# Optimization experiments

Hardware: AMD Instinct MI355X
Metric: run time of the kernel (lower is better)

The kernel has to match this reference:

```python
import jax, jax.numpy as jnp
import numpy as np

Q_DIM = 32
HID = 512
OFF = Q_DIM * (Q_DIM - 1) // 2  # 496 strictly-lower-triangular entries


def setup_inputs() -> dict:
    key = jax.random.key(0)
    ks = jax.random.split(key, 20)

    def w(k, shape, fan_in):
        return (jax.random.normal(k, shape, jnp.float32) / np.float32(np.sqrt(fan_in)))

    return {
        "q": jax.random.normal(ks[0], (1, Q_DIM), jnp.float32),
        "q_t": jax.random.normal(ks[1], (1, Q_DIM), jnp.float32),
        "q_tt": jax.random.normal(ks[2], (1, Q_DIM), jnp.float32),
        # L-network (torch Linear convention: y = x @ W.T + b)
        "W1": w(ks[3], (HID, Q_DIM), Q_DIM), "b1": jnp.zeros((HID,), jnp.float32),
        "W2": w(ks[4], (HID, HID), HID),     "b2": jnp.zeros((HID,), jnp.float32),
        "W3": w(ks[5], (HID, HID), HID),     "b3": jnp.zeros((HID,), jnp.float32),
        "Wd": w(ks[6], (Q_DIM, HID), HID),   "bd": jnp.zeros((Q_DIM,), jnp.float32),
        "Wo": w(ks[7], (OFF, HID), HID),     "bo": jnp.zeros((OFF,), jnp.float32),
        # g-network
        "Wg1": w(ks[8], (HID, Q_DIM), Q_DIM), "bg1": jnp.zeros((HID,), jnp.float32),
        "Wg2": w(ks[9], (HID, HID), HID),     "bg2": jnp.zeros((HID,), jnp.float32),
        "Wg3": w(ks[10], (Q_DIM, HID), HID),  "bg3": jnp.zeros((Q_DIM,), jnp.float32),
    }


def reference(q, q_t, q_tt, W1, b1, W2, b2, W3, b3, Wd, bd, Wo, bo,
              Wg1, bg1, Wg2, bg2, Wg3, bg3):
    n = Q_DIM
    # L-network forward (sigmoid MLP)
    h1 = jax.nn.sigmoid(q @ W1.T + b1)    # [1, 512]
    h2 = jax.nn.sigmoid(h1 @ W2.T + b2)   # [1, 512]
    h3 = jax.nn.sigmoid(h2 @ W3.T + b3)   # [1, 512]
    l_diag = jnp.exp(h3 @ Wd.T + bd)      # [1, n]
    l_off = h3 @ Wo.T + bo                # [1, OFF]

    # Assemble lower-triangular L. The torch loop fills the strictly-lower
    # triangle in row-major order: (1,0),(2,0),(2,1),(3,0),... == tril_indices(k=-1).
    rows, cols = jnp.tril_indices(n, -1)
    ar = jnp.arange(n)
    L = (jnp.zeros((n, n), q.dtype)
         .at[ar, ar].set(l_diag[0])
         .at[rows, cols].set(l_off[0]))

    # Analytic Jacobian chain. diag_embed(s) @ W == s[:,None] * W (row scaling).
    s1 = (h1 * (1.0 - h1))[0]             # sigmoid'
    s2 = (h2 * (1.0 - h2))[0]
    s3 = (h3 * (1.0 - h3))[0]
    dh1 = s1[:, None] * W1                # [512, n]
    dh2 = s2[:, None] * W2                # [512, 512]
    dh3 = s3[:, None] * W3                # [512, 512]
    dh4 = jnp.concatenate([l_diag[0][:, None] * Wd, Wo], axis=0)  # [n+OFF, 512]
    dl_dq = dh4 @ (dh3 @ (dh2 @ dh1))     # [n+OFF, n]

    # dL_dq[i, j, k] = d L[i,j] / d q_k  (same tril assembly, vectorized over k)
    dL_dq = (jnp.zeros((n, n, n), q.dtype)
             .at[ar, ar, :].set(dl_dq[:n])
             .at[rows, cols, :].set(dl_dq[n:]))

    qt_col = q_t.T                        # [n, 1]
    Dqt = jnp.einsum('ijk,k->ij', dL_dq, q_t[0])   # comp_3_1 / squeeze pattern
    Fjk = jnp.einsum('ijk,i->jk', dL_dq, q_t[0])   # comp_4_1 pattern
    LTqt = L.T @ qt_col                   # [n, 1]

    comp_1 = L @ (L.T @ q_tt.T)
    comp_2 = L @ (Dqt.T @ qt_col)
    comp_3 = Dqt @ LTqt
    comp_4 = Fjk @ LTqt
    comp_5 = (q_t @ (L @ Dqt.T)).T

    # g-network
    g1 = jax.nn.sigmoid(q @ Wg1.T + bg1)
    g2 = jax.nn.sigmoid(g1 @ Wg2.T + bg2)
    g = (g2 @ Wg3.T + bg3).reshape(n, 1)

    tau = comp_1 + comp_2 + comp_3 - 0.5 * comp_4 - 0.5 * comp_5 + g
    return tau.T                          # [1, n]
```

## Files before the change

kernel.cpp:

```cpp
#include <hip/hip_runtime.h>
#include <cmath>

#define NQ 32
#define H 512
#define NOFF 496
#define NR4 528
#define NBLK 34

__device__ __forceinline__ float sigmoidf(float x) {
    return 1.0f / (1.0f + __expf(-x));
}
__device__ __forceinline__ float dot4(float4 a, float4 b) {
    return a.x * b.x + a.y * b.y + a.z * b.z + a.w * b.w;
}
__device__ __forceinline__ float ldagent(const float* p) {
    return __hip_atomic_load(p, __ATOMIC_RELAXED, __HIP_MEMORY_SCOPE_AGENT);
}
__device__ __forceinline__ float red16(float a) {
    a += __shfl_xor(a, 1, 64);
    a += __shfl_xor(a, 2, 64);
    a += __shfl_xor(a, 4, 64);
    a += __shfl_xor(a, 8, 64);
    return a;
}

__global__ void __launch_bounds__(1024, 1) fused(
    const float* __restrict__ q, const float* __restrict__ q_t, const float* __restrict__ q_tt,
    const float* __restrict__ W1, const float* __restrict__ b1,
    const float* __restrict__ W2, const float* __restrict__ b2,
    const float* __restrict__ W3, const float* __restrict__ b3,
    const float* __restrict__ Wd, const float* __restrict__ bd,
    const float* __restrict__ Wo, const float* __restrict__ bo,
    const float* __restrict__ Wg1, const float* __restrict__ bg1,
    const float* __restrict__ Wg2, const float* __restrict__ bg2,
    const float* __restrict__ Wg3, const float* __restrict__ bg3,
    float* __restrict__ U, float* __restrict__ gvec,
    unsigned* __restrict__ done, float* __restrict__ out)
{
    const int c = blockIdx.x;
    const int tid = threadIdx.x;
    const int lane = tid & 63, w = tid >> 6;
    const int p = lane & 15, rg = lane >> 4;
    const bool isg = (c == NBLK - 1);

    __shared__ float qs[NQ];
    __shared__ float hv[H], bvv[H], hv2[H], bv2[H];
    __shared__ float ldiag[NQ], loff[NOFF], vv[NR4];
    __shared__ float Lm[NQ][NQ + 1], Dq[NQ][NQ + 1], Fj[NQ][NQ + 1];
    __shared__ float qts[NQ], qtts[NQ], LTq[NQ], t1s[NQ], u2[NQ];
    __shared__ int amLast;

    if (tid < NQ) qs[tid] = q[tid];
    __syncthreads();

    if (tid < H) {
        const float* Wf = isg ? Wg1 : W1;
        const float* bf = isg ? bg1 : b1;
        const float4* wr = (const float4*)(Wf + tid * NQ);
        float acc = 0.f;
        #pragma unroll
        for (int cc = 0; cc < 8; ++cc) {
            float4 wv4 = wr[cc];
            acc += wv4.x * qs[4*cc] + wv4.y * qs[4*cc+1] + wv4.z * qs[4*cc+2] + wv4.w * qs[4*cc+3];
        }
        float h = sigmoidf(acc + bf[tid]);
        hv[tid] = h;
        bvv[tid] = (c == 0 || isg) ? h : h * (1.f - h) * Wf[tid * NQ + (c - 1)];
    }
    __syncthreads();

    {
        const float4* hv4 = (const float4*)hv;
        const float4* bv4 = (const float4*)bvv;
        float4 bh[8], bb[8];
        #pragma unroll
        for (int i = 0; i < 8; ++i) { bh[i] = hv4[p + 16*i]; bb[i] = bv4[p + 16*i]; }
        const float4* Wv = (const float4*)(isg ? Wg2 : W2);
        const float* bias = isg ? bg2 : b2;
        #pragma unroll 2
        for (int pass = 0; pass < 8; ++pass) {
            int r = w * 32 + pass * 4 + rg;
            const float4* wr = Wv + (size_t)r * (H / 4);
            float4 wreg[8];
            #pragma unroll
            for (int i = 0; i < 8; ++i) wreg[i] = wr[p + 16*i];
            float aH = 0.f, aB = 0.f;
            #pragma unroll
            for (int i = 0; i < 8; ++i) { aH += dot4(wreg[i], bh[i]); aB += dot4(wreg[i], bb[i]); }
            aH = red16(aH);
            aB = red16(aB);
            if (p == 0) {
                float h2 = sigmoidf(aH + bias[r]);
                hv2[r] = h2;
                bv2[r] = (c == 0 || isg) ? h2 : h2 * (1.f - h2) * aB;
            }
        }
    }
    __syncthreads();

    if (!isg) {
        const float4* hv4 = (const float4*)hv2;
        const float4* bv4 = (const float4*)bv2;
        float4 bh[8], bb[8];
        #pragma unroll
        for (int i = 0; i < 8; ++i) { bh[i] = hv4[p + 16*i]; bb[i] = bv4[p + 16*i]; }
        #pragma unroll 2
        for (int pass = 0; pass < 8; ++pass) {
            int r = w * 32 + pass * 4 + rg;
            const float4* wr = (const float4*)W3 + (size_t)r * (H / 4);
            float4 wreg[8];
            #pragma unroll
            for (int i = 0; i < 8; ++i) wreg[i] = wr[p + 16*i];
            float aH = 0.f, aB = 0.f;
            #pragma unroll
            for (int i = 0; i < 8; ++i) { aH += dot4(wreg[i], bh[i]); aB += dot4(wreg[i], bb[i]); }
            aH = red16(aH);
            aB = red16(aB);
            if (p == 0) {
                float h3 = sigmoidf(aH + b3[r]);
                hv[r] = h3;
                bvv[r] = (c == 0) ? h3 : h3 * (1.f - h3) * aB;
            }
        }
    } else {
        const float4* hv4 = (const float4*)hv2;
        float4 bh[8];
        #pragma unroll
        for (int i = 0; i < 8; ++i) bh[i] = hv4[p + 16*i];
        if (w < 8) {
            int r = w * 4 + rg;
            const float4* wr = (const float4*)Wg3 + (size_t)r * (H / 4);
            float4 wreg[8];
            #pragma unroll
            for (int i = 0; i < 8; ++i) wreg[i] = wr[p + 16*i];
            float aH = 0.f;
            #pragma unroll
            for (int i = 0; i < 8; ++i) aH += dot4(wreg[i], bh[i]);
            aH = red16(aH);
            if (p == 0) gvec[r] = aH + bg3[r];
        }
    }
    __syncthreads();

    if (!isg) {
        const float4* bv4 = (const float4*)bvv;
        float4 bb[8];
        #pragma unroll
        for (int i = 0; i < 8; ++i) bb[i] = bv4[p + 16*i];
        #pragma unroll 2
        for (int pass = 0; pass < 9; ++pass) {
            int r = pass * 64 + w * 4 + rg;
            if (r < NR4) {
                const float4* wr = (r < NQ) ? ((const float4*)Wd + (size_t)r * (H / 4))
                                            : ((const float4*)Wo + (size_t)(r - NQ) * (H / 4));
                float4 wreg[8];
                #pragma unroll
                for (int i = 0; i < 8; ++i) wreg[i] = wr[p + 16*i];
                float aB = 0.f;
                #pragma unroll
                for (int i = 0; i < 8; ++i) aB += dot4(wreg[i], bb[i]);
                aB = red16(aB);
                if (p == 0) U[c * NR4 + r] = aB;
            }
        }
    }

    __threadfence();
    __syncthreads();
    if (tid == 0) {
        unsigned old = __hip_atomic_fetch_add(done, 1u, __ATOMIC_ACQ_REL, __HIP_MEMORY_SCOPE_AGENT);
        amLast = (old == NBLK - 1) ? 1 : 0;
    }
    __syncthreads();
    if (!amLast) return;

    if (tid < NQ) {
        ldiag[tid] = __expf(ldagent(&U[tid]) + bd[tid]);
        qts[tid]  = q_t[tid];
        qtts[tid] = q_tt[tid];
    }
    for (int r = tid; r < NOFF; r += 1024)
        loff[r] = ldagent(&U[NQ + r]) + bo[r];
    __syncthreads();
    for (int m = tid; m < NR4; m += 1024) {
        float acc = 0.f;
        #pragma unroll
        for (int kk = 0; kk < NQ; ++kk)
            acc += ldagent(&U[(kk + 1) * NR4 + m]) * qts[kk];
        vv[m] = (m < NQ) ? ldiag[m] * acc : acc;
    }
    for (int pp = tid; pp < NQ * NQ; pp += 1024) {
        int i = pp >> 5, j = pp & 31;
        Lm[i][j] = (i == j) ? ldiag[i]
                 : (j < i ? loff[i * (i - 1) / 2 + j] : 0.f);
    }
    for (int pp = tid; pp < NQ * NQ; pp += 1024) {
        int j = pp >> 5, kk = pp & 31;
        const float* Uc = U + (kk + 1) * NR4;
        float acc = qts[j] * ldiag[j] * ldagent(&Uc[j]);
        for (int i = j + 1; i < NQ; ++i)
            acc += qts[i] * ldagent(&Uc[NQ + i * (i - 1) / 2 + j]);
        Fj[j][kk] = acc;
    }
    __syncthreads();
    for (int pp = tid; pp < NQ * NQ; pp += 1024) {
        int i = pp >> 5, j = pp & 31;
        Dq[i][j] = (i == j) ? vv[i]
                 : (j < i ? vv[NQ + i * (i - 1) / 2 + j] : 0.f);
    }
    if (tid < NQ) {
        int kcol = tid;
        float a = 0.f, bsum = 0.f;
        #pragma unroll
        for (int j = 0; j < NQ; ++j) {
            a    += Lm[j][kcol] * qts[j];
            bsum += Lm[j][kcol] * qtts[j];
        }
        LTq[kcol] = a;
        t1s[kcol] = bsum;
    }
    __syncthreads();
    if (tid < NQ) {
        int kcol = tid;
        float a = 0.f;
        #pragma unroll
        for (int j = 0; j < NQ; ++j) a += Dq[j][kcol] * qts[j];
        u2[kcol] = a;
    }
    __syncthreads();
    if (tid < NQ) {
        int i = tid;
        float c1 = 0.f, c2 = 0.f, c3 = 0.f, c4 = 0.f;
        #pragma unroll
        for (int kk = 0; kk < NQ; ++kk) {
            c1 += Lm[i][kk] * t1s[kk];
            c2 += Lm[i][kk] * u2[kk];
            c3 += Dq[i][kk] * LTq[kk];
            c4 += Fj[i][kk] * LTq[kk];
        }
        out[i] = c1 + c2 + 0.5f * c3 - 0.5f * c4 + ldagent(&gvec[i]);
    }
}

extern "C" void kernel_launch(void* const* d_in, const int* in_sizes, int n_in,
                              void* d_out, int out_size, void* d_ws, size_t ws_size,
                              hipStream_t stream) {
    const float* q    = (const float*)d_in[0];
    const float* q_t  = (const float*)d_in[1];
    const float* q_tt = (const float*)d_in[2];
    const float* W1   = (const float*)d_in[3];
    const float* b1   = (const float*)d_in[4];
    const float* W2   = (const float*)d_in[5];
    const float* b2   = (const float*)d_in[6];
    const float* W3   = (const float*)d_in[7];
    const float* b3   = (const float*)d_in[8];
    const float* Wd   = (const float*)d_in[9];
    const float* bd   = (const float*)d_in[10];
    const float* Wo   = (const float*)d_in[11];
    const float* bo   = (const float*)d_in[12];
    const float* Wg1  = (const float*)d_in[13];
    const float* bg1  = (const float*)d_in[14];
    const float* Wg2  = (const float*)d_in[15];
    const float* bg2  = (const float*)d_in[16];
    const float* Wg3  = (const float*)d_in[17];
    const float* bg3  = (const float*)d_in[18];

    float* ws = (float*)d_ws;
    float* U       = ws;
    float* gvec    = ws + 17424;
    unsigned* done = (unsigned*)(ws + 17456);
    float* out     = (float*)d_out;

    hipMemsetAsync(done, 0, sizeof(unsigned), stream);
    hipLaunchKernelGGL(fused, dim3(NBLK), dim3(1024), 0, stream,
                       q, q_t, q_tt, W1, b1, W2, b2, W3, b3,
                       Wd, bd, Wo, bo, Wg1, bg1, Wg2, bg2, Wg3, bg3,
                       U, gvec, done, out);
}
```

Before: 151.0 us.

## Split fused kernel into three layer kernels spread across 8x more blocks

Replaces the single 34-block kernel, in which each block runs the whole three-layer chain for one Jacobian column, with three kernels (ka, kb, kc). Each kernel splits a layer's output rows into 8 row blocks per column, giving 264 to 272 blocks of 256 threads. This spreads the weight-streaming matvecs across far more compute units. Layer activations and Jacobian columns now round-trip through global workspace between launches, and the forward value and the derivative products are computed in separate passes. The cost is two extra kernel launches plus the intermediate global traffic.

```diff
diff --git a/kernel.cpp b/kernel.cpp
--- a/kernel.cpp
+++ b/kernel.cpp
@@ -5,7 +5,6 @@
 #define H 512
 #define NOFF 496
 #define NR4 528
-#define NBLK 34
 
 __device__ __forceinline__ float sigmoidf(float x) {
     return 1.0f / (1.0f + __expf(-x));
@@ -24,143 +23,179 @@
     return a;
 }
 
-__global__ void __launch_bounds__(1024, 1) fused(
-    const float* __restrict__ q, const float* __restrict__ q_t, const float* __restrict__ q_tt,
+__global__ void __launch_bounds__(256) ka(
+    const float* __restrict__ q,
     const float* __restrict__ W1, const float* __restrict__ b1,
     const float* __restrict__ W2, const float* __restrict__ b2,
-    const float* __restrict__ W3, const float* __restrict__ b3,
-    const float* __restrict__ Wd, const float* __restrict__ bd,
-    const float* __restrict__ Wo, const float* __restrict__ bo,
     const float* __restrict__ Wg1, const float* __restrict__ bg1,
     const float* __restrict__ Wg2, const float* __restrict__ bg2,
-    const float* __restrict__ Wg3, const float* __restrict__ bg3,
-    float* __restrict__ U, float* __restrict__ gvec,
-    unsigned* __restrict__ done, float* __restrict__ out)
+    float* __restrict__ Y, float* __restrict__ g2)
 {
-    const int c = blockIdx.x;
+    const int c = blockIdx.x >> 3, rb = blockIdx.x & 7;
     const int tid = threadIdx.x;
     const int lane = tid & 63, w = tid >> 6;
     const int p = lane & 15, rg = lane >> 4;
-    const bool isg = (c == NBLK - 1);
+    const bool isg = (c == 33);
 
     __shared__ float qs[NQ];
-    __shared__ float hv[H], bvv[H], hv2[H], bv2[H];
+    __shared__ float bcol[H];
+
+    if (tid < NQ) qs[tid] = q[tid];
+    __syncthreads();
+
+    const float* Wf = isg ? Wg1 : W1;
+    const float* bf = isg ? bg1 : b1;
+    for (int j = tid; j < H; j += 256) {
+        const float4* wr = (const float4*)(Wf + j * NQ);
+        float acc = 0.f;
+        #pragma unroll
+        for (int cc = 0; cc < 8; ++cc) {
+            float4 wv = wr[cc];
+            acc += wv.x * qs[4*cc] + wv.y * qs[4*cc+1] + wv.z * qs[4*cc+2] + wv.w * qs[4*cc+3];
+        }
+        float h = sigmoidf(acc + bf[j]);
+        bcol[j] = (c == 0 || isg) ? h : h * (1.f - h) * Wf[j * NQ + (c - 1)];
+    }
+    __syncthreads();
+
+    const float4* b4 = (const float4*)bcol;
+    float4 bb[8];
+    #pragma unroll
+    for (int i = 0; i < 8; ++i) bb[i] = b4[p + 16 * i];
+
+    const float4* Wv = (const float4*)(isg ? Wg2 : W2);
+    const int r0 = rb * 64;
+    #pragma unroll 2
+    for (int pass = 0; pass < 4; ++pass) {
+        int r = r0 + pass * 16 + w * 4 + rg;
+        const float4* wr = Wv + (size_t)r * (H / 4);
+        float4 wreg[8];
+        #pragma unroll
+        for (int i = 0; i < 8; ++i) wreg[i] = wr[p + 16 * i];
+        float a = 0.f;
+        #pragma unroll
+        for (int i = 0; i < 8; ++i) a += dot4(wreg[i], bb[i]);
+        a = red16(a);
+        if (p == 0) {
+            if (c == 0)      Y[r] = sigmoidf(a + b2[r]);
+            else if (!isg)   Y[c * H + r] = a;
+            else             g2[r] = sigmoidf(a + bg2[r]);
+        }
+    }
+}
+
+__global__ void __launch_bounds__(256) kb(
+    const float* __restrict__ W3, const float* __restrict__ b3,
+    const float* __restrict__ Wg3, const float* __restrict__ bg3,
+    const float* __restrict__ Y, const float* __restrict__ g2,
+    float* __restrict__ Z, float* __restrict__ gvec)
+{
+    const int tid = threadIdx.x;
+    const int lane = tid & 63, w = tid >> 6;
+    const int p = lane & 15, rg = lane >> 4;
+
+    if (blockIdx.x == 264) {
+        const float4* g4 = (const float4*)g2;
+        float4 bb[8];
+        #pragma unroll
+        for (int i = 0; i < 8; ++i) bb[i] = g4[p + 16 * i];
+        #pragma unroll
+        for (int pass = 0; pass < 2; ++pass) {
+            int r = pass * 16 + w * 4 + rg;
+            const float4* wr = (const float4*)Wg3 + (size_t)r * (H / 4);
+            float4 wreg[8];
+            #pragma unroll
+            for (int i = 0; i < 8; ++i) wreg[i] = wr[p + 16 * i];
+            float a = 0.f;
+            #pragma unroll
+            for (int i = 0; i < 8; ++i) a += dot4(wreg[i], bb[i]);
+            a = red16(a);
+            if (p == 0) gvec[r] = a + bg3[r];
+        }
+        return;
+    }
+
+    const int c = blockIdx.x >> 3, rb = blockIdx.x & 7;
+    const float4* Y0 = (const float4*)Y;
+    const float4* Yc = (const float4*)(Y + c * H);
+    float4 bb[8];
+    #pragma unroll
+    for (int i = 0; i < 8; ++i) {
+        float4 h = Y0[p + 16 * i];
+        if (c == 0) bb[i] = h;
+        else {
+            float4 yc = Yc[p + 16 * i];
+            bb[i] = make_float4(h.x*(1.f-h.x)*yc.x, h.y*(1.f-h.y)*yc.y,
+                                h.z*(1.f-h.z)*yc.z, h.w*(1.f-h.w)*yc.w);
+        }
+    }
+    const int r0 = rb * 64;
+    #pragma unroll 2
+    for (int pass = 0; pass < 4; ++pass) {
+        int r = r0 + pass * 16 + w * 4 + rg;
+        const float4* wr = (const float4*)W3 + (size_t)r * (H / 4);
+        float4 wreg[8];
+        #pragma unroll
+        for (int i = 0; i < 8; ++i) wreg[i] = wr[p + 16 * i];
+        float a = 0.f;
+        #pragma unroll
+        for (int i = 0; i < 8; ++i) a += dot4(wreg[i], bb[i]);
+        a = red16(a);
+        if (p == 0) {
+            if (c == 0) Z[r] = sigmoidf(a + b3[r]);
+            else        Z[c * H + r] = a;
+        }
+    }
+}
+
+__global__ void __launch_bounds__(256) kc(
+    const float* __restrict__ Wd, const float* __restrict__ bd,
+    const float* __restrict__ Wo, const float* __restrict__ bo,
+    const float* __restrict__ Z,
+    const float* __restrict__ q_t, const float* __restrict__ q_tt,
+    const float* __restrict__ gvec,
+    float* __restrict__ U, unsigned* __restrict__ done,
+    float* __restrict__ out)
+{
+    const int c = blockIdx.x >> 3, rb = blockIdx.x & 7;
+    const int tid = threadIdx.x;
+    const int lane = tid & 63, w = tid >> 6;
+    const int p = lane & 15, rg = lane >> 4;
+
     __shared__ float ldiag[NQ], loff[NOFF], vv[NR4];
     __shared__ float Lm[NQ][NQ + 1], Dq[NQ][NQ + 1], Fj[NQ][NQ + 1];
     __shared__ float qts[NQ], qtts[NQ], LTq[NQ], t1s[NQ], u2[NQ];
     __shared__ int amLast;
 
-    if (tid < NQ) qs[tid] = q[tid];
-    __syncthreads();
-
-    if (tid < H) {
-        const float* Wf = isg ? Wg1 : W1;
-        const float* bf = isg ? bg1 : b1;
-        const float4* wr = (const float4*)(Wf + tid * NQ);
-        float acc = 0.f;
-        #pragma unroll
-        for (int cc = 0; cc < 8; ++cc) {
-            float4 wv4 = wr[cc];
-            acc += wv4.x * qs[4*cc] + wv4.y * qs[4*cc+1] + wv4.z * qs[4*cc+2] + wv4.w * qs[4*cc+3];
-        }
-        float h = sigmoidf(acc + bf[tid]);
-        hv[tid] = h;
-        bvv[tid] = (c == 0 || isg) ? h : h * (1.f - h) * Wf[tid * NQ + (c - 1)];
-    }
-    __syncthreads();
-
     {
-        const float4* hv4 = (const float4*)hv;
-        const float4* bv4 = (const float4*)bvv;
-        float4 bh[8], bb[8];
-        #pragma unroll
-        for (int i = 0; i < 8; ++i) { bh[i] = hv4[p + 16*i]; bb[i] = bv4[p + 16*i]; }
-        const float4* Wv = (const float4*)(isg ? Wg2 : W2);
-        const float* bias = isg ? bg2 : b2;
+        const float4* Z0 = (const float4*)Z;
+        const float4* Zc = (const float4*)(Z + c * H);
+        float4 bb[8];
+        #pragma unroll
+        for (int i = 0; i < 8; ++i) {
+            float4 h = Z0[p + 16 * i];
+            if (c == 0) bb[i] = h;
+            else {
+                float4 zc = Zc[p + 16 * i];
+                bb[i] = make_float4(h.x*(1.f-h.x)*zc.x, h.y*(1.f-h.y)*zc.y,
+                                    h.z*(1.f-h.z)*zc.z, h.w*(1.f-h.w)*zc.w);
+            }
+        }
         #pragma unroll 2
-        for (int pass = 0; pass < 8; ++pass) {
-            int r = w * 32 + pass * 4 + rg;
-            const float4* wr = Wv + (size_t)r * (H / 4);
-            float4 wreg[8];
-            #pragma unroll
-            for (int i = 0; i < 8; ++i) wreg[i] = wr[p + 16*i];
-            float aH = 0.f, aB = 0.f;
-            #pragma unroll
-            for (int i = 0; i < 8; ++i) { aH += dot4(wreg[i], bh[i]); aB += dot4(wreg[i], bb[i]); }
-            aH = red16(aH);
-            aB = red16(aB);
-            if (p == 0) {
-                float h2 = sigmoidf(aH + bias[r]);
-                hv2[r] = h2;
-                bv2[r] = (c == 0 || isg) ? h2 : h2 * (1.f - h2) * aB;
-            }
-        }
-    }
-    __syncthreads();
-
-    if (!isg) {
-        const float4* hv4 = (const float4*)hv2;
-        const float4* bv4 = (const float4*)bv2;
-        float4 bh[8], bb[8];
-        #pragma unroll
-        for (int i = 0; i < 8; ++i) { bh[i] = hv4[p + 16*i]; bb[i] = bv4[p + 16*i]; }
-        #pragma unroll 2
-        for (int pass = 0; pass < 8; ++pass) {
-            int r = w * 32 + pass * 4 + rg;
-            const float4* wr = (const float4*)W3 + (size_t)r * (H / 4);
-            float4 wreg[8];
-            #pragma unroll
-            for (int i = 0; i < 8; ++i) wreg[i] = wr[p + 16*i];
-            float aH = 0.f, aB = 0.f;
-            #pragma unroll
-            for (int i = 0; i < 8; ++i) { aH += dot4(wreg[i], bh[i]); aB += dot4(wreg[i], bb[i]); }
-            aH = red16(aH);
-            aB = red16(aB);
-            if (p == 0) {
-                float h3 = sigmoidf(aH + b3[r]);
-                hv[r] = h3;
-                bvv[r] = (c == 0) ? h3 : h3 * (1.f - h3) * aB;
-            }
-        }
-    } else {
-        const float4* hv4 = (const float4*)hv2;
-        float4 bh[8];
-        #pragma unroll
-        for (int i = 0; i < 8; ++i) bh[i] = hv4[p + 16*i];
-        if (w < 8) {
-            int r = w * 4 + rg;
-            const float4* wr = (const float4*)Wg3 + (size_t)r * (H / 4);
-            float4 wreg[8];
-            #pragma unroll
-            for (int i = 0; i < 8; ++i) wreg[i] = wr[p + 16*i];
-            float aH = 0.f;
-            #pragma unroll
-            for (int i = 0; i < 8; ++i) aH += dot4(wreg[i], bh[i]);
-            aH = red16(aH);
-            if (p == 0) gvec[r] = aH + bg3[r];
-        }
-    }
-    __syncthreads();
-
-    if (!isg) {
-        const float4* bv4 = (const float4*)bvv;
-        float4 bb[8];
-        #pragma unroll
-        for (int i = 0; i < 8; ++i) bb[i] = bv4[p + 16*i];
-        #pragma unroll 2
-        for (int pass = 0; pass < 9; ++pass) {
-            int r = pass * 64 + w * 4 + rg;
-            if (r < NR4) {
+        for (int pass = 0; pass < 5; ++pass) {
+            int idx = pass * 16 + w * 4 + rg;
+            if (idx < 66) {
+                int r = rb * 66 + idx;
                 const float4* wr = (r < NQ) ? ((const float4*)Wd + (size_t)r * (H / 4))
                                             : ((const float4*)Wo + (size_t)(r - NQ) * (H / 4));
                 float4 wreg[8];
                 #pragma unroll
-                for (int i = 0; i < 8; ++i) wreg[i] = wr[p + 16*i];
-                float aB = 0.f;
+                for (int i = 0; i < 8; ++i) wreg[i] = wr[p + 16 * i];
+                float a = 0.f;
                 #pragma unroll
-                for (int i = 0; i < 8; ++i) aB += dot4(wreg[i], bb[i]);
-                aB = red16(aB);
-                if (p == 0) U[c * NR4 + r] = aB;
+                for (int i = 0; i < 8; ++i) a += dot4(wreg[i], bb[i]);
+                a = red16(a);
+                if (p == 0) U[c * NR4 + r] = a;
             }
         }
     }
@@ -169,7 +204,7 @@
     __syncthreads();
     if (tid == 0) {
         unsigned old = __hip_atomic_fetch_add(done, 1u, __ATOMIC_ACQ_REL, __HIP_MEMORY_SCOPE_AGENT);
-        amLast = (old == NBLK - 1) ? 1 : 0;
+        amLast = (old == 263u) ? 1 : 0;
     }
     __syncthreads();
     if (!amLast) return;
@@ -179,22 +214,22 @@
         qts[tid]  = q_t[tid];
         qtts[tid] = q_tt[tid];
     }
-    for (int r = tid; r < NOFF; r += 1024)
+    for (int r = tid; r < NOFF; r += 256)
         loff[r] = ldagent(&U[NQ + r]) + bo[r];
     __syncthreads();
-    for (int m = tid; m < NR4; m += 1024) {
+    for (int m = tid; m < NR4; m += 256) {
         float acc = 0.f;
         #pragma unroll
         for (int kk = 0; kk < NQ; ++kk)
             acc += ldagent(&U[(kk + 1) * NR4 + m]) * qts[kk];
         vv[m] = (m < NQ) ? ldiag[m] * acc : acc;
     }
-    for (int pp = tid; pp < NQ * NQ; pp += 1024) {
+    for (int pp = tid; pp < NQ * NQ; pp += 256) {
         int i = pp >> 5, j = pp & 31;
         Lm[i][j] = (i == j) ? ldiag[i]
                  : (j < i ? loff[i * (i - 1) / 2 + j] : 0.f);
     }
-    for (int pp = tid; pp < NQ * NQ; pp += 1024) {
+    for (int pp = tid; pp < NQ * NQ; pp += 256) {
         int j = pp >> 5, kk = pp & 31;
         const float* Uc = U + (kk + 1) * NR4;
         float acc = qts[j] * ldiag[j] * ldagent(&Uc[j]);
@@ -203,7 +238,7 @@
         Fj[j][kk] = acc;
     }
     __syncthreads();
-    for (int pp = tid; pp < NQ * NQ; pp += 1024) {
+    for (int pp = tid; pp < NQ * NQ; pp += 256) {
         int i = pp >> 5, j = pp & 31;
         Dq[i][j] = (i == j) ? vv[i]
                  : (j < i ? vv[NQ + i * (i - 1) / 2 + j] : 0.f);
@@ -238,7 +273,7 @@
             c3 += Dq[i][kk] * LTq[kk];
             c4 += Fj[i][kk] * LTq[kk];
         }
-        out[i] = c1 + c2 + 0.5f * c3 - 0.5f * c4 + ldagent(&gvec[i]);
+        out[i] = c1 + c2 + 0.5f * c3 - 0.5f * c4 + gvec[i];
     }
 }
 
@@ -266,14 +301,19 @@
     const float* bg3  = (const float*)d_in[18];
 
     float* ws = (float*)d_ws;
-    float* U       = ws;
-    float* gvec    = ws + 17424;
-    unsigned* done = (unsigned*)(ws + 17456);
+    float* Y       = ws;
+    float* g2      = ws + 16896;
+    float* Z       = ws + 17408;
+    float* gvec    = ws + 34304;
+    float* U       = ws + 34336;
+    unsigned* done = (unsigned*)(ws + 51760);
     float* out     = (float*)d_out;
 
     hipMemsetAsync(done, 0, sizeof(unsigned), stream);
-    hipLaunchKernelGGL(fused, dim3(NBLK), dim3(1024), 0, stream,
-                       q, q_t, q_tt, W1, b1, W2, b2, W3, b3,
-                       Wd, bd, Wo, bo, Wg1, bg1, Wg2, bg2, Wg3, bg3,
-                       U, gvec, done, out);
-}
+    hipLaunchKernelGGL(ka, dim3(272), dim3(256), 0, stream,
+                       q, W1, b1, W2, b2, Wg1, bg1, Wg2, bg2, Y, g2);
+    hipLaunchKernelGGL(kb, dim3(265), dim3(256), 0, stream,
+                       W3, b3, Wg3, bg3, Y, g2, Z, gvec);
+    hipLaunchKernelGGL(kc, dim3(264), dim3(256), 0, stream,
+                       Wd, bd, Wo, bo, Z, q_t, q_tt, gvec, U, done, out);
+}
```

After: 155.0 us. 1.03x slower.
